# Optimization experiments

Measured on AMD Instinct MI355X. Metric: run time of the kernel, lower is better.

## Reference

```python
import jax, jax.numpy as jnp
import numpy as np

MARGIN = 0.3
LOSS_FLOOR = 1e-06


def setup_inputs() -> dict:
    key = jax.random.key(0)
    k1, k2 = jax.random.split(key)
    embeddings = jax.random.normal(k1, (8192, 128), dtype=jnp.float32)
    labels = jax.random.randint(k2, (8192,), 0, 512, dtype=jnp.int64)
    return {"embeddings": embeddings, "labels": labels}


def _pairwise_dist(x):
    # Euclidean cdist via the GEMM identity; clamp for numerical safety.
    sq = jnp.sum(x * x, axis=1)  # [N]
    d2 = sq[:, None] + sq[None, :] - 2.0 * (x @ x.T)  # [N, N]
    return jnp.sqrt(jnp.maximum(d2, 1e-12))


def reference(embeddings, labels):
    dist = _pairwise_dist(embeddings)  # [N, N]
    same = labels[None, :] == labels[:, None]  # [N, N]
    n = embeddings.shape[0]
    eye = jnp.eye(n, dtype=bool)
    mask_pos = same & ~eye
    mask_neg = ~same  # diagonal is same-label, so already excluded

    neg_inf = jnp.float32(-jnp.inf)
    pos_inf = jnp.float32(jnp.inf)
    hardest_pos = jnp.max(jnp.where(mask_pos, dist, neg_inf), axis=1)  # [N]
    hardest_neg = jnp.min(jnp.where(mask_neg, dist, pos_inf), axis=1)  # [N]

    valid = jnp.any(mask_pos, axis=1) & jnp.any(mask_neg, axis=1)  # [N]
    per_row = jnp.maximum(hardest_pos - hardest_neg + MARGIN, LOSS_FLOOR)
    num_valid = jnp.sum(valid)
    total = jnp.sum(jnp.where(valid, per_row, 0.0))
    return jnp.where(num_valid > 0, total / jnp.maximum(num_valid, 1), 0.0).astype(embeddings.dtype)
```

## Files before the change

### kernel.cpp

```cpp
#include <hip/hip_runtime.h>
#include <math.h>


#define NROWS 8192
#define DIM   128
#define JSPLIT 64
#define JCHUNK (NROWS / JSPLIT)
#define NSUB   4
#define SUBROWS 32

typedef short bf16x8 __attribute__((ext_vector_type(8)));
typedef float f32x4  __attribute__((ext_vector_type(4)));

static __device__ __forceinline__ unsigned short f2bf(float f) {
    unsigned u = __float_as_uint(f);
    unsigned r = (u + 0x7FFFu + ((u >> 16) & 1u)) >> 16;
    return (unsigned short)r;
}

static __device__ __forceinline__ unsigned encf(float f) {
    unsigned u = __float_as_uint(f);
    return (u & 0x80000000u) ? ~u : (u | 0x80000000u);
}
static __device__ __forceinline__ float decf(unsigned e) {
    unsigned u = (e & 0x80000000u) ? (e & 0x7FFFFFFFu) : ~e;
    return __uint_as_float(u);
}
#define ENC_PINF 0xFF800000u
#define ENC_NINF 0x007FFFFFu

static __device__ __forceinline__ void gload_lds16(const void* g, void* l) {
    __builtin_amdgcn_global_load_lds(
        (const __attribute__((address_space(1))) unsigned int*)g,
        (__attribute__((address_space(3))) unsigned int*)l, 16, 0, 0);
}

__global__ __launch_bounds__(256) void prep_kernel(
    const float* __restrict__ x, float* __restrict__ sqp,
    float* __restrict__ sqh, unsigned* __restrict__ hpE,
    unsigned* __restrict__ hnE, unsigned short* __restrict__ xb,
    float* __restrict__ gsum, float* __restrict__ gcnt,
    unsigned* __restrict__ done) {
    int t = blockIdx.x * 256 + threadIdx.x;
    int row = t >> 5;
    int c = t & 31;
    float4 v = ((const float4*)x)[t];
    float ps = v.x * v.x + v.y * v.y + v.z * v.z + v.w * v.w;
#pragma unroll
    for (int s = 1; s < 32; s <<= 1) ps += __shfl_xor(ps, s, 64);
    if (c == 0) {
        sqp[row] = ps;
        sqh[row] = -0.5f * ps;
    } else if (c == 1) {
        hpE[row] = ENC_PINF;
    } else if (c == 2) {
        hnE[row] = ENC_NINF;
    } else if (t == 3) {
        *gsum = 0.f; *gcnt = 0.f; *done = 0u;
    }
    ushort4 ob;
    ob.x = f2bf(v.x); ob.y = f2bf(v.y); ob.z = f2bf(v.z); ob.w = f2bf(v.w);
    ((ushort4*)xb)[t] = ob;
}

__global__ __launch_bounds__(256, 4) void pair_kernel(
    const unsigned short* __restrict__ xb, const float* __restrict__ sqh,
    const int* __restrict__ labels,
    unsigned* __restrict__ hpE, unsigned* __restrict__ hnE) {
    __shared__ __attribute__((aligned(16))) unsigned char abuf[2][SUBROWS * 256];
    __shared__ __attribute__((aligned(16))) float sqs[JCHUNK];
    __shared__ __attribute__((aligned(16))) int labs[JCHUNK];

    const int tid = threadIdx.x;
    const int lane = tid & 63;
    const int wid = tid >> 6;
    const int q = lane >> 4;
    const int r = lane & 15;
    const int ibase = blockIdx.x * 256 + wid * 64;
    const int jbase = blockIdx.y * JCHUNK;

    if (tid < JCHUNK) {
        sqs[tid] = sqh[jbase + tid];
        labs[tid] = labels[jbase + tid];
    }

    bf16x8 bfrag[4][4];
    int labi[4];
#pragma unroll
    for (int sub = 0; sub < 4; ++sub) {
        int irow = ibase + sub * 16 + r;
        labi[sub] = labels[irow];
#pragma unroll
        for (int ks = 0; ks < 4; ++ks)
            bfrag[sub][ks] = *(const bf16x8*)(xb + (size_t)irow * DIM + ks * 32 + q * 8);
    }

    float hp[4] = {INFINITY, INFINITY, INFINITY, INFINITY};
    float hn[4] = {-INFINITY, -INFINITY, -INFINITY, -INFINITY};

    auto stage = [&](int s, int buf) {
        const char* gb = (const char*)xb + (size_t)(jbase + s * SUBROWS) * 256;
        unsigned char* lb = &abuf[buf][0];
#pragma unroll
        for (int p = 0; p < 2; ++p) {
            int row = wid * 8 + p * 4 + (lane >> 4);
            int colb = (lane & 15) * 16;
            const void* g = gb + row * 256 + (colb ^ ((row & 15) << 4));
            void* l = lb + wid * 2048 + p * 1024;
            gload_lds16(g, l);
        }
    };

    auto compute_tile = [&](int s, int buf, int t) {
        const unsigned char* lb = &abuf[buf][0];
        const int tt = s * 2 + t;
        bf16x8 af[4];
        const int rowb = (t * 16 + r) * 256;
        const int sw = r << 4;
#pragma unroll
        for (int ks = 0; ks < 4; ++ks)
            af[ks] = *(const bf16x8*)(lb + rowb + ((ks * 64 + q * 16) ^ sw));
        f32x4 ci = *(const f32x4*)(&sqs[tt * 16 + q * 4]);
        int4 labj = *(const int4*)(labs + tt * 16 + q * 4);
#pragma unroll
        for (int sub = 0; sub < 4; ++sub) {
            f32x4 acc = ci;
            acc = __builtin_amdgcn_mfma_f32_16x16x32_bf16(af[0], bfrag[sub][0], acc, 0, 0, 0);
            acc = __builtin_amdgcn_mfma_f32_16x16x32_bf16(af[1], bfrag[sub][1], acc, 0, 0, 0);
            acc = __builtin_amdgcn_mfma_f32_16x16x32_bf16(af[2], bfrag[sub][2], acc, 0, 0, 0);
            acc = __builtin_amdgcn_mfma_f32_16x16x32_bf16(af[3], bfrag[sub][3], acc, 0, 0, 0);
            const int li = labi[sub];
            float u0 = acc[0], u1 = acc[1], u2 = acc[2], u3 = acc[3];
            hp[sub] = fminf(hp[sub], (labj.x == li) ? u0 : INFINITY);
            hn[sub] = fmaxf(hn[sub], (labj.x == li) ? -INFINITY : u0);
            hp[sub] = fminf(hp[sub], (labj.y == li) ? u1 : INFINITY);
            hn[sub] = fmaxf(hn[sub], (labj.y == li) ? -INFINITY : u1);
            hp[sub] = fminf(hp[sub], (labj.z == li) ? u2 : INFINITY);
            hn[sub] = fmaxf(hn[sub], (labj.z == li) ? -INFINITY : u2);
            hp[sub] = fminf(hp[sub], (labj.w == li) ? u3 : INFINITY);
            hn[sub] = fmaxf(hn[sub], (labj.w == li) ? -INFINITY : u3);
        }
    };

    stage(0, 0);
    __syncthreads();
#pragma unroll
    for (int s = 0; s < NSUB; ++s) {
        if (s + 1 < NSUB) stage(s + 1, (s + 1) & 1);
#pragma unroll
        for (int t = 0; t < 2; ++t) compute_tile(s, s & 1, t);
        __syncthreads();
    }

#pragma unroll
    for (int sub = 0; sub < 4; ++sub) {
        hp[sub] = fminf(hp[sub], __shfl_xor(hp[sub], 16, 64));
        hp[sub] = fminf(hp[sub], __shfl_xor(hp[sub], 32, 64));
        hn[sub] = fmaxf(hn[sub], __shfl_xor(hn[sub], 16, 64));
        hn[sub] = fmaxf(hn[sub], __shfl_xor(hn[sub], 32, 64));
    }
    if (lane < 16) {
#pragma unroll
        for (int sub = 0; sub < 4; ++sub) {
            int irow = ibase + sub * 16 + lane;
            unsigned ep = encf(hp[sub]);
            if (ep != ENC_PINF) atomicMin(&hpE[irow], ep);
            unsigned en = encf(hn[sub]);
            if (en != ENC_NINF) atomicMax(&hnE[irow], en);
        }
    }
}

__global__ __launch_bounds__(256) void reduce_kernel(
    const unsigned* __restrict__ hpE, const unsigned* __restrict__ hnE,
    const float* __restrict__ sqp, float* __restrict__ gsum,
    float* __restrict__ gcnt, unsigned* __restrict__ done,
    float* __restrict__ out) {
    int row = blockIdx.x * 256 + threadIdx.x;
    unsigned hpv = hpE[row];
    unsigned hnv = hnE[row];
    float s = sqp[row];
    float sum = 0.f, cnt = 0.f;
    if (hpv != ENC_PINF && hnv != ENC_NINF) {
        float dp = sqrtf(fmaxf(s - 2.f * decf(hpv), 1e-12f));
        float dn = sqrtf(fmaxf(s - 2.f * decf(hnv), 1e-12f));
        sum = fmaxf(dp - dn + 0.3f, 1e-6f);
        cnt = 1.f;
    }
#pragma unroll
    for (int sh = 1; sh < 64; sh <<= 1) {
        sum += __shfl_xor(sum, sh, 64);
        cnt += __shfl_xor(cnt, sh, 64);
    }
    __shared__ float ss[4], sc[4];
    int w = threadIdx.x >> 6;
    if ((threadIdx.x & 63) == 0) { ss[w] = sum; sc[w] = cnt; }
    __syncthreads();
    if (threadIdx.x == 0) {
        atomicAdd(gsum, ss[0] + ss[1] + ss[2] + ss[3]);
        atomicAdd(gcnt, sc[0] + sc[1] + sc[2] + sc[3]);
        __threadfence();
        unsigned t = atomicAdd(done, 1u);
        if (t == gridDim.x - 1) {
            float S = atomicAdd(gsum, 0.f);
            float C = atomicAdd(gcnt, 0.f);
            out[0] = (C > 0.f) ? S / C : 0.f;
        }
    }
}

extern "C" void kernel_launch(void* const* d_in, const int* in_sizes, int n_in,
                              void* d_out, int out_size, void* d_ws, size_t ws_size,
                              hipStream_t stream) {
    const float* x = (const float*)d_in[0];
    const int* labels = (const int*)d_in[1];
    float* out = (float*)d_out;

    char* ws = (char*)d_ws;
    float* gsum = (float*)ws;
    float* gcnt = (float*)(ws + 4);
    unsigned* done = (unsigned*)(ws + 8);
    float* sqp = (float*)(ws + 4096);
    float* sqh = (float*)(ws + 36864);
    unsigned* hpE = (unsigned*)(ws + 69632);
    unsigned* hnE = (unsigned*)(ws + 102400);
    unsigned short* xb = (unsigned short*)(ws + 135168);

    prep_kernel<<<(NROWS * 32) / 256, 256, 0, stream>>>(
        x, sqp, sqh, hpE, hnE, xb, gsum, gcnt, done);
    pair_kernel<<<dim3(NROWS / 256, JSPLIT), 256, 0, stream>>>(
        xb, sqh, labels, hpE, hnE);
    reduce_kernel<<<NROWS / 256, 256, 0, stream>>>(
        hpE, hnE, sqp, gsum, gcnt, done, out);
}
```

Before: 89.72 us.

## Fuse final reduction into pair kernel via last-block-done counter

Removes the separate reduce kernel launch. Each pair block increments a global counter after its atomics, and the last block reads the per-row hardest values through atomics and computes the mean loss. It also restructures the masked min/max into tree reductions to shorten dependency chains. In exchange, the final reduction over all rows now runs serially in a single block, and every block pays a threadfence plus one atomic.

```diff
diff --git a/kernel.cpp b/kernel.cpp
--- a/kernel.cpp
+++ b/kernel.cpp
@@ -8,6 +8,7 @@
 #define JCHUNK (NROWS / JSPLIT)
 #define NSUB   4
 #define SUBROWS 32
+#define NBLK   (32 * JSPLIT)
 
 typedef short bf16x8 __attribute__((ext_vector_type(8)));
 typedef float f32x4  __attribute__((ext_vector_type(4)));
@@ -39,7 +40,6 @@
     const float* __restrict__ x, float* __restrict__ sqp,
     float* __restrict__ sqh, unsigned* __restrict__ hpE,
     unsigned* __restrict__ hnE, unsigned short* __restrict__ xb,
-    float* __restrict__ gsum, float* __restrict__ gcnt,
     unsigned* __restrict__ done) {
     int t = blockIdx.x * 256 + threadIdx.x;
     int row = t >> 5;
@@ -56,7 +56,7 @@
     } else if (c == 2) {
         hnE[row] = ENC_NINF;
     } else if (t == 3) {
-        *gsum = 0.f; *gcnt = 0.f; *done = 0u;
+        *done = 0u;
     }
     ushort4 ob;
     ob.x = f2bf(v.x); ob.y = f2bf(v.y); ob.z = f2bf(v.z); ob.w = f2bf(v.w);
@@ -65,11 +65,14 @@
 
 __global__ __launch_bounds__(256, 4) void pair_kernel(
     const unsigned short* __restrict__ xb, const float* __restrict__ sqh,
-    const int* __restrict__ labels,
-    unsigned* __restrict__ hpE, unsigned* __restrict__ hnE) {
+    const float* __restrict__ sqp, const int* __restrict__ labels,
+    unsigned* __restrict__ hpE, unsigned* __restrict__ hnE,
+    unsigned* __restrict__ done, float* __restrict__ out) {
     __shared__ __attribute__((aligned(16))) unsigned char abuf[2][SUBROWS * 256];
     __shared__ __attribute__((aligned(16))) float sqs[JCHUNK];
     __shared__ __attribute__((aligned(16))) int labs[JCHUNK];
+    __shared__ int isLast;
+    __shared__ float ss[4], sc[4];
 
     const int tid = threadIdx.x;
     const int lane = tid & 63;
@@ -130,15 +133,16 @@
             acc = __builtin_amdgcn_mfma_f32_16x16x32_bf16(af[2], bfrag[sub][2], acc, 0, 0, 0);
             acc = __builtin_amdgcn_mfma_f32_16x16x32_bf16(af[3], bfrag[sub][3], acc, 0, 0, 0);
             const int li = labi[sub];
-            float u0 = acc[0], u1 = acc[1], u2 = acc[2], u3 = acc[3];
-            hp[sub] = fminf(hp[sub], (labj.x == li) ? u0 : INFINITY);
-            hn[sub] = fmaxf(hn[sub], (labj.x == li) ? -INFINITY : u0);
-            hp[sub] = fminf(hp[sub], (labj.y == li) ? u1 : INFINITY);
-            hn[sub] = fmaxf(hn[sub], (labj.y == li) ? -INFINITY : u1);
-            hp[sub] = fminf(hp[sub], (labj.z == li) ? u2 : INFINITY);
-            hn[sub] = fmaxf(hn[sub], (labj.z == li) ? -INFINITY : u2);
-            hp[sub] = fminf(hp[sub], (labj.w == li) ? u3 : INFINITY);
-            hn[sub] = fmaxf(hn[sub], (labj.w == li) ? -INFINITY : u3);
+            float m0 = (labj.x == li) ? acc[0] : INFINITY;
+            float m1 = (labj.y == li) ? acc[1] : INFINITY;
+            float m2 = (labj.z == li) ? acc[2] : INFINITY;
+            float m3 = (labj.w == li) ? acc[3] : INFINITY;
+            hp[sub] = fminf(hp[sub], fminf(fminf(m0, m1), fminf(m2, m3)));
+            float n0 = (labj.x == li) ? -INFINITY : acc[0];
+            float n1 = (labj.y == li) ? -INFINITY : acc[1];
+            float n2 = (labj.z == li) ? -INFINITY : acc[2];
+            float n3 = (labj.w == li) ? -INFINITY : acc[3];
+            hn[sub] = fmaxf(hn[sub], fmaxf(fmaxf(n0, n1), fmaxf(n2, n3)));
         }
     };
 
@@ -169,43 +173,38 @@
             if (en != ENC_NINF) atomicMax(&hnE[irow], en);
         }
     }
-}
-
-__global__ __launch_bounds__(256) void reduce_kernel(
-    const unsigned* __restrict__ hpE, const unsigned* __restrict__ hnE,
-    const float* __restrict__ sqp, float* __restrict__ gsum,
-    float* __restrict__ gcnt, unsigned* __restrict__ done,
-    float* __restrict__ out) {
-    int row = blockIdx.x * 256 + threadIdx.x;
-    unsigned hpv = hpE[row];
-    unsigned hnv = hnE[row];
-    float s = sqp[row];
+
+    __threadfence();
+    if (tid == 0) {
+        unsigned t = atomicAdd(done, 1u);
+        isLast = (t == NBLK - 1);
+    }
+    __syncthreads();
+    if (!isLast) return;
+
     float sum = 0.f, cnt = 0.f;
-    if (hpv != ENC_PINF && hnv != ENC_NINF) {
-        float dp = sqrtf(fmaxf(s - 2.f * decf(hpv), 1e-12f));
-        float dn = sqrtf(fmaxf(s - 2.f * decf(hnv), 1e-12f));
-        sum = fmaxf(dp - dn + 0.3f, 1e-6f);
-        cnt = 1.f;
+    for (int row = tid; row < NROWS; row += 256) {
+        unsigned hpv = atomicMin(&hpE[row], 0xFFFFFFFFu);
+        unsigned hnv = atomicMax(&hnE[row], 0u);
+        float s = sqp[row];
+        if (hpv != ENC_PINF && hnv != ENC_NINF) {
+            float dp = sqrtf(fmaxf(s - 2.f * decf(hpv), 1e-12f));
+            float dn = sqrtf(fmaxf(s - 2.f * decf(hnv), 1e-12f));
+            sum += fmaxf(dp - dn + 0.3f, 1e-6f);
+            cnt += 1.f;
+        }
     }
 #pragma unroll
     for (int sh = 1; sh < 64; sh <<= 1) {
         sum += __shfl_xor(sum, sh, 64);
         cnt += __shfl_xor(cnt, sh, 64);
     }
-    __shared__ float ss[4], sc[4];
-    int w = threadIdx.x >> 6;
-    if ((threadIdx.x & 63) == 0) { ss[w] = sum; sc[w] = cnt; }
+    if ((tid & 63) == 0) { ss[tid >> 6] = sum; sc[tid >> 6] = cnt; }
     __syncthreads();
-    if (threadIdx.x == 0) {
-        atomicAdd(gsum, ss[0] + ss[1] + ss[2] + ss[3]);
-        atomicAdd(gcnt, sc[0] + sc[1] + sc[2] + sc[3]);
-        __threadfence();
-        unsigned t = atomicAdd(done, 1u);
-        if (t == gridDim.x - 1) {
-            float S = atomicAdd(gsum, 0.f);
-            float C = atomicAdd(gcnt, 0.f);
-            out[0] = (C > 0.f) ? S / C : 0.f;
-        }
+    if (tid == 0) {
+        float S = ss[0] + ss[1] + ss[2] + ss[3];
+        float C = sc[0] + sc[1] + sc[2] + sc[3];
+        out[0] = (C > 0.f) ? S / C : 0.f;
     }
 }
 
@@ -217,9 +216,7 @@
     float* out = (float*)d_out;
 
     char* ws = (char*)d_ws;
-    float* gsum = (float*)ws;
-    float* gcnt = (float*)(ws + 4);
-    unsigned* done = (unsigned*)(ws + 8);
+    unsigned* done = (unsigned*)ws;
     float* sqp = (float*)(ws + 4096);
     float* sqh = (float*)(ws + 36864);
     unsigned* hpE = (unsigned*)(ws + 69632);
@@ -227,9 +224,7 @@
     unsigned short* xb = (unsigned short*)(ws + 135168);
 
     prep_kernel<<<(NROWS * 32) / 256, 256, 0, stream>>>(
-        x, sqp, sqh, hpE, hnE, xb, gsum, gcnt, done);
+        x, sqp, sqh, hpE, hnE, xb, done);
     pair_kernel<<<dim3(NROWS / 256, JSPLIT), 256, 0, stream>>>(
-        xb, sqh, labels, hpE, hnE);
-    reduce_kernel<<<NROWS / 256, 256, 0, stream>>>(
-        hpE, hnE, sqp, gsum, gcnt, done, out);
-}
+        xb, sqh, sqp, labels, hpE, hnE, done, out);
+}
```

Result: slower. 339.4 us (+278.3%).
